# Kernel tuning notes

Hardware: AMD Instinct MI355X
Metric: run time of the kernel (lower is better)

Reference implementation:

```python
import jax, jax.numpy as jnp
import numpy as np

N_EMBD = 1024
N_HEAD = 16
HEAD_DIM = N_EMBD // N_HEAD


def setup_inputs() -> dict:
    key = jax.random.key(0)
    ks = jax.random.split(key, 5)
    scale = 0.02
    x = jax.random.normal(ks[0], (2, 2048, N_EMBD), dtype=jnp.float32)
    w_attn = jax.random.normal(ks[1], (N_EMBD, 3 * N_EMBD), dtype=jnp.float32) * scale
    b_attn = jax.random.normal(ks[2], (3 * N_EMBD,), dtype=jnp.float32) * scale
    w_proj = jax.random.normal(ks[3], (N_EMBD, N_EMBD), dtype=jnp.float32) * scale
    b_proj = jax.random.normal(ks[4], (N_EMBD,), dtype=jnp.float32) * scale
    return {"x": x, "w_attn": w_attn, "b_attn": b_attn, "w_proj": w_proj, "b_proj": b_proj}


def reference(x, w_attn, b_attn, w_proj, b_proj):
    B, T, C = x.shape
    qkv = x @ w_attn + b_attn  # [B,T,3C]
    q, k, v = jnp.split(qkv, 3, axis=-1)
    # [B, H, T, D]
    q = q.reshape(B, T, N_HEAD, HEAD_DIM).transpose(0, 2, 1, 3)
    k = k.reshape(B, T, N_HEAD, HEAD_DIM).transpose(0, 2, 1, 3)
    v = v.reshape(B, T, N_HEAD, HEAD_DIM).transpose(0, 2, 1, 3)
    att = jnp.einsum("bhqd,bhkd->bhqk", q, k) * (1.0 / np.sqrt(HEAD_DIM))
    causal = jnp.tril(jnp.ones((T, T), dtype=bool))
    att = jnp.where(causal[None, None], att, jnp.float32(-jnp.inf))
    att = jax.nn.softmax(att, axis=-1)
    y = jnp.einsum("bhqk,bhkd->bhqd", att, v)  # [B,H,T,D]
    y = y.transpose(0, 2, 1, 3).reshape(B, T, C)
    return y @ w_proj + b_proj
```

## Files before the change

### kernel.cpp

```cpp
#include <hip/hip_runtime.h>
#include <stdint.h>

#define SEQ   2048
#define EMBD  1024
#define M_ROWS 4096

typedef unsigned short u16;
typedef unsigned int u32;
typedef __attribute__((ext_vector_type(8))) short bf16x8;
typedef __attribute__((ext_vector_type(4))) float f32x4;

__device__ __forceinline__ u16 f2b(float f) {
  u32 x = __float_as_uint(f);
  return (u16)((x + 0x7FFFu + ((x >> 16) & 1u)) >> 16);
}

__device__ __forceinline__ u32 pkbf(float a, float b) {
  u32 r;
  asm("v_cvt_pk_bf16_f32 %0, %1, %2" : "=v"(r) : "v"(a), "v"(b));
  return r;
}

__device__ __forceinline__ float exp2fast(float x) {
#if __has_builtin(__builtin_amdgcn_exp2f)
  return __builtin_amdgcn_exp2f(x);
#else
  return __expf(x * 0.69314718f);
#endif
}

__device__ __forceinline__ float rcpfast(float x) {
#if __has_builtin(__builtin_amdgcn_rcpf)
  return __builtin_amdgcn_rcpf(x);
#else
  return 1.f / x;
#endif
}

#define AS1(p) ((const __attribute__((address_space(1))) void*)(uintptr_t)(p))
#define AS3(p) ((__attribute__((address_space(3))) void*)(uintptr_t)(p))

__global__ __launch_bounds__(256) void cvt_f32_bf16(
    const float* __restrict__ in, u16* __restrict__ out, int n8) {
  int i = blockIdx.x * 256 + threadIdx.x;
  if (i >= n8) return;
  const float4* p = (const float4*)in + 2 * (size_t)i;
  float4 a = p[0], b = p[1];
  uint4 o;
  o.x = (u32)f2b(a.x) | ((u32)f2b(a.y) << 16);
  o.y = (u32)f2b(a.z) | ((u32)f2b(a.w) << 16);
  o.z = (u32)f2b(b.x) | ((u32)f2b(b.y) << 16);
  o.w = (u32)f2b(b.z) | ((u32)f2b(b.w) << 16);
  ((uint4*)out)[i] = o;
}

__global__ __launch_bounds__(256) void transpose_cvt2(
    const float* __restrict__ wa, u16* __restrict__ wat,
    const float* __restrict__ wp, u16* __restrict__ wpt) {
  __shared__ float t[64][65];
  const int bxr = blockIdx.x;
  const float* w = (bxr < 48) ? wa : wp;
  u16* wt = (bxr < 48) ? wat : wpt;
  const int N = (bxr < 48) ? 3072 : 1024;
  const int bx = (bxr < 48) ? bxr : bxr - 48;
  const int K = 1024;
  const int n0 = bx * 64, k0 = blockIdx.y * 64;
  const int c = threadIdx.x & 63, r4 = threadIdx.x >> 6;
#pragma unroll
  for (int j = 0; j < 16; ++j) {
    const int r = j * 4 + r4;
    t[c][r] = w[(size_t)(k0 + r) * N + n0 + c];
  }
  __syncthreads();
#pragma unroll
  for (int j = 0; j < 16; ++j) {
    const int nr = j * 4 + r4;
    wt[(size_t)(n0 + nr) * K + k0 + c] = f2b(t[nr][c]);
  }
}

template <bool OUT_BF16>
__global__ __launch_bounds__(256) void gemm_kmajor(
    const u16* __restrict__ A, const u16* __restrict__ Bt,
    const float* __restrict__ bias, void* __restrict__ outp,
    int M, int N, int K, int nbx) {
  __shared__ __align__(16) u16 sm[2][2][128 * 32];

  const int nwg = gridDim.x;
  const int qq = nwg >> 3, rr = nwg & 7;
  const int xcd = blockIdx.x & 7, off = blockIdx.x >> 3;
  const int wgid = (xcd < rr ? xcd * (qq + 1) : rr * (qq + 1) + (xcd - rr) * qq) + off;
  const int bx = wgid % nbx, by = wgid / nbx;
  const int row0 = by * 128, col0 = bx * 128;

  const int tid = threadIdx.x;
  const int w = tid >> 6, lane = tid & 63;
  const int wrow = (w >> 1) * 64, wcol = (w & 1) * 64;

  f32x4 acc[4][4];
#pragma unroll
  for (int a = 0; a < 4; ++a)
#pragma unroll
    for (int b = 0; b < 4; ++b)
#pragma unroll
      for (int e = 0; e < 4; ++e) acc[a][b][e] = 0.f;

  const size_t Kb = (size_t)K * 2;

  auto stage = [&](int k0, int buf) {
#pragma unroll
    for (int c = 0; c < 4; ++c) {
      const int ch = w * 4 + c;
      const int i = ch & 7;
      const int rloc = i * 16 + (lane >> 2);
      const int kb = ((lane & 3) * 16) ^ ((rloc & 3) << 4);
      const u16* mat = (ch < 8) ? A : Bt;
      const int r0 = (ch < 8) ? row0 : col0;
      const char* src = (const char*)mat + (size_t)(r0 + rloc) * Kb + k0 * 2 + kb;
      char* dst = (char*)&sm[buf][(ch < 8) ? 0 : 1][0] + i * 1024;
      __builtin_amdgcn_global_load_lds(AS1(src), AS3(dst), 16, 0, 0);
    }
  };

  auto compute = [&](int buf) {
    bf16x8 af[4], bfr[4];
    const char* As = (const char*)&sm[buf][0][0];
    const char* Bs = (const char*)&sm[buf][1][0];
#pragma unroll
    for (int rb = 0; rb < 4; ++rb) {
      const int rl = wrow + rb * 16 + (lane & 15);
      const int kb2 = ((lane >> 4) * 16) ^ ((rl & 3) << 4);
      af[rb] = *(const bf16x8*)(As + rl * 64 + kb2);
    }
#pragma unroll
    for (int cb = 0; cb < 4; ++cb) {
      const int rl = wcol + cb * 16 + (lane & 15);
      const int kb2 = ((lane >> 4) * 16) ^ ((rl & 3) << 4);
      bfr[cb] = *(const bf16x8*)(Bs + rl * 64 + kb2);
    }
#pragma unroll
    for (int rb = 0; rb < 4; ++rb)
#pragma unroll
      for (int cb = 0; cb < 4; ++cb)
        acc[rb][cb] = __builtin_amdgcn_mfma_f32_16x16x32_bf16(
            af[rb], bfr[cb], acc[rb][cb], 0, 0, 0);
  };

  const int nt = K >> 5;
  stage(0, 0);
  int cur = 0;
  for (int t = 0; t < nt - 1; ++t) {
    __syncthreads();
    stage((t + 1) * 32, cur ^ 1);
    compute(cur);
    cur ^= 1;
  }
  __syncthreads();
  compute(cur);

#pragma unroll
  for (int cb = 0; cb < 4; ++cb) {
    const int colg = col0 + wcol + cb * 16 + (lane & 15);
    const float bv = bias[colg];
#pragma unroll
    for (int rb = 0; rb < 4; ++rb) {
#pragma unroll
      for (int i = 0; i < 4; ++i) {
        const int rowg = row0 + wrow + rb * 16 + (lane >> 4) * 4 + i;
        const float v = acc[rb][cb][i] + bv;
        if (OUT_BF16) {
          const u32 hv = f2b(v);
          const u32 pv = (u32)__shfl_xor((int)hv, 1);
          if (!(lane & 1))
            *(u32*)((u16*)outp + (size_t)rowg * N + colg) = hv | (pv << 16);
        } else {
          ((float*)outp)[(size_t)rowg * N + colg] = v;
        }
      }
    }
  }
}

__global__ __launch_bounds__(256, 2) void attn_mfma2(
    const u16* __restrict__ qkvb, u16* __restrict__ yb) {
  __shared__ __align__(16) char lds[32768];

  const int bx = blockIdx.x;
  const int pr = bx >> 5;
  const int bh = bx & 31;
  const int bb = bh >> 4, h = bh & 15;

  const int tid = threadIdx.x;
  const int w = tid >> 6, lane = tid & 63;
  const int hh = lane >> 4, qh = lane & 15;

  const size_t rowb = 6144;
  const char* base = (const char*)qkvb + (size_t)bb * SEQ * rowb;
  const int koffb = EMBD * 2 + h * 128;
  const int voffb = 2 * EMBD * 2 + h * 128;

  const int krow_in_chunk = lane >> 3;
  const int vkv = (tid & 31) * 2;
  const int vdg = tid >> 5;

  for (int half = 0; half < 2; ++half) {
    const int qt = half ? pr : 31 - pr;
    const int q_abs = qt * 64 + w * 16 + qh;
    const int qloc = w * 16 + qh;

    const char* qp = base + (size_t)q_abs * rowb + h * 128 + hh * 16;
    const bf16x8 qf0 = *(const bf16x8*)qp;
    const bf16x8 qf1 = *(const bf16x8*)(qp + 64);

    float m2 = -1e30f, l = 0.f;
    f32x4 of[4];
#pragma unroll
    for (int db = 0; db < 4; ++db)
#pragma unroll
      for (int e = 0; e < 4; ++e) of[db][e] = 0.f;

    {
#pragma unroll
      for (int cc = 0; cc < 2; ++cc) {
        const int i = w * 2 + cc;
        const int kvl = i * 8 + krow_in_chunk;
        const int gs = (lane & 7) ^ ((i & 3) | ((krow_in_chunk & 1) << 2));
        const char* src = base + (size_t)kvl * rowb + koffb + gs * 16;
        __builtin_amdgcn_global_load_lds(AS1(src), AS3(lds + i * 1024), 16, 0, 0);
      }
      const char* vp = base + (size_t)vkv * rowb + voffb + vdg * 16;
      uint4 va = *(const uint4*)vp;
      uint4 vb = *(const uint4*)(vp + rowb);
      union { uint4 q; u16 s[8]; } ua, ub;
      ua.q = va; ub.q = vb;
      u32* vt = (u32*)(lds + 16384);
#pragma unroll
      for (int e = 0; e < 8; ++e) {
        const int d = vdg * 8 + e;
        vt[d * 32 + ((vkv >> 1) ^ ((d & 7) << 2))] =
            (u32)ua.s[e] | ((u32)ub.s[e] << 16);
      }
    }
    __syncthreads();

    for (int kt = 0; kt <= qt; ++kt) {
      const int cur = kt & 1;
      const char* ksb = lds + cur * 8192;
      const char* vtb = lds + 16384 + cur * 8192;

      uint4 va, vb;
      const bool pref = (kt < qt);
      if (pref) {
#pragma unroll
        for (int cc = 0; cc < 2; ++cc) {
          const int i = w * 2 + cc;
          const int kvl = i * 8 + krow_in_chunk;
          const int gs = (lane & 7) ^ ((i & 3) | ((krow_in_chunk & 1) << 2));
          const char* src =
              base + (size_t)((kt + 1) * 64 + kvl) * rowb + koffb + gs * 16;
          __builtin_amdgcn_global_load_lds(
              AS1(src), AS3(lds + (cur ^ 1) * 8192 + i * 1024), 16, 0, 0);
        }
        const char* vp =
            base + (size_t)((kt + 1) * 64 + vkv) * rowb + voffb + vdg * 16;
        va = *(const uint4*)vp;
        vb = *(const uint4*)(vp + rowb);
      }

      f32x4 st[4];
      __builtin_amdgcn_s_setprio(1);
#pragma unroll
      for (int rb = 0; rb < 4; ++rb) {
#pragma unroll
        for (int e = 0; e < 4; ++e) st[rb][e] = 0.f;
        const int kv = 32 * (rb >> 1) + 8 * ((lane >> 2) & 3) + 4 * (rb & 1) +
                       (lane & 3);
        const int f = ((kv >> 3) & 3) | ((kv & 1) << 2);
        const char* rp = ksb + kv * 128;
        const bf16x8 k0 = *(const bf16x8*)(rp + ((hh * 16) ^ (f << 4)));
        const bf16x8 k1 = *(const bf16x8*)(rp + ((64 + hh * 16) ^ (f << 4)));
        st[rb] = __builtin_amdgcn_mfma_f32_16x16x32_bf16(k0, qf0, st[rb], 0, 0, 0);
        st[rb] = __builtin_amdgcn_mfma_f32_16x16x32_bf16(k1, qf1, st[rb], 0, 0, 0);
      }
      __builtin_amdgcn_s_setprio(0);

      const float C = 0.18033688f;
      float pmax = -3.0e38f;
      if (kt == qt) {
#pragma unroll
        for (int rb = 0; rb < 4; ++rb) {
          const int kvb = 32 * (rb >> 1) + 8 * hh + 4 * (rb & 1);
#pragma unroll
          for (int i = 0; i < 4; ++i) {
            float v = st[rb][i] * C;
            if (kvb + i > qloc) v = -3.0e38f;
            st[rb][i] = v;
            pmax = fmaxf(pmax, v);
          }
        }
      } else {
#pragma unroll
        for (int rb = 0; rb < 4; ++rb)
#pragma unroll
          for (int i = 0; i < 4; ++i) {
            const float v = st[rb][i] * C;
            st[rb][i] = v;
            pmax = fmaxf(pmax, v);
          }
      }
      pmax = fmaxf(pmax, __shfl_xor(pmax, 16));
      pmax = fmaxf(pmax, __shfl_xor(pmax, 32));

      if (__any(pmax > m2 + 5.f)) {
        const float mn = fmaxf(m2, pmax);
        const float al = exp2fast(m2 - mn);
        m2 = mn;
        l *= al;
#pragma unroll
        for (int db = 0; db < 4; ++db)
#pragma unroll
          for (int e = 0; e < 4; ++e) of[db][e] *= al;
      }

      float ls = 0.f;
#pragma unroll
      for (int rb = 0; rb < 4; ++rb)
#pragma unroll
        for (int i = 0; i < 4; ++i) {
          const float p = exp2fast(st[rb][i] - m2);
          st[rb][i] = p;
          ls += p;
        }
      ls += __shfl_xor(ls, 16);
      ls += __shfl_xor(ls, 32);
      l += ls;

      union { u32 wd[4]; bf16x8 v; } pf0, pf1;
      pf0.wd[0] = pkbf(st[0][0], st[0][1]);
      pf0.wd[1] = pkbf(st[0][2], st[0][3]);
      pf0.wd[2] = pkbf(st[1][0], st[1][1]);
      pf0.wd[3] = pkbf(st[1][2], st[1][3]);
      pf1.wd[0] = pkbf(st[2][0], st[2][1]);
      pf1.wd[1] = pkbf(st[2][2], st[2][3]);
      pf1.wd[2] = pkbf(st[3][0], st[3][1]);
      pf1.wd[3] = pkbf(st[3][2], st[3][3]);

      __builtin_amdgcn_s_setprio(1);
#pragma unroll
      for (int db = 0; db < 4; ++db) {
        const int d = db * 16 + qh;
        const int g = d & 7;
        const char* rp = vtb + d * 128;
        const bf16x8 v0 = *(const bf16x8*)(rp + ((hh * 16) ^ (g << 4)));
        const bf16x8 v1 = *(const bf16x8*)(rp + ((64 + hh * 16) ^ (g << 4)));
        of[db] = __builtin_amdgcn_mfma_f32_16x16x32_bf16(v0, pf0.v, of[db], 0, 0, 0);
        of[db] = __builtin_amdgcn_mfma_f32_16x16x32_bf16(v1, pf1.v, of[db], 0, 0, 0);
      }
      __builtin_amdgcn_s_setprio(0);

      if (pref) {
        union { uint4 q; u16 s[8]; } ua, ub;
        ua.q = va; ub.q = vb;
        u32* vt = (u32*)(lds + 16384 + (cur ^ 1) * 8192);
#pragma unroll
        for (int e = 0; e < 8; ++e) {
          const int d = vdg * 8 + e;
          vt[d * 32 + ((vkv >> 1) ^ ((d & 7) << 2))] =
              (u32)ua.s[e] | ((u32)ub.s[e] << 16);
        }
      }
      __syncthreads();
    }

    const float inv = rcpfast(l);
    u16* yrow = yb + (size_t)(bb * SEQ + q_abs) * EMBD + h * 64;
#pragma unroll
    for (int db = 0; db < 4; ++db) {
      const u32 w0 = pkbf(of[db][0] * inv, of[db][1] * inv);
      const u32 w1 = pkbf(of[db][2] * inv, of[db][3] * inv);
      *(u32*)(yrow + db * 16 + 4 * hh) = w0;
      *(u32*)(yrow + db * 16 + 4 * hh + 2) = w1;
    }
    __syncthreads();
  }
}

extern "C" void kernel_launch(void* const* d_in, const int* in_sizes, int n_in,
                              void* d_out, int out_size, void* d_ws,
                              size_t ws_size, hipStream_t stream) {
  const float* x      = (const float*)d_in[0];
  const float* w_attn = (const float*)d_in[1];
  const float* b_attn = (const float*)d_in[2];
  const float* w_proj = (const float*)d_in[3];
  const float* b_proj = (const float*)d_in[4];
  float* out = (float*)d_out;

  u16* xb   = (u16*)d_ws;
  u16* wat  = xb + (size_t)M_ROWS * EMBD;
  u16* wpt  = wat + (size_t)3 * EMBD * EMBD;
  u16* qkvb = wpt + (size_t)EMBD * EMBD;
  u16* yb   = qkvb + (size_t)M_ROWS * 3 * EMBD;

  cvt_f32_bf16<<<(M_ROWS * EMBD / 8 + 255) / 256, 256, 0, stream>>>(
      x, xb, M_ROWS * EMBD / 8);
  transpose_cvt2<<<dim3(64, 16), 256, 0, stream>>>(w_attn, wat, w_proj, wpt);

  gemm_kmajor<true><<<768, 256, 0, stream>>>(
      xb, wat, b_attn, qkvb, M_ROWS, 3 * EMBD, EMBD, 24);

  attn_mfma2<<<512, 256, 0, stream>>>(qkvb, yb);

  gemm_kmajor<false><<<256, 256, 0, stream>>>(
      yb, wpt, b_proj, out, M_ROWS, EMBD, EMBD, 8);
}
```

Baseline: 188.2 us.

## Split attention into one block per query tile with XCD-aware mapping; fuse prep kernels

The attention kernel now launches one block per (batch-head, query tile) instead of pairing two query tiles per block. Block indices are remapped so each XCD handles a fixed set of heads, which keeps K/V reuse within one L2, and launch bounds allow four blocks per CU. The x conversion and weight transpose kernels are merged into one launch. In exchange, causal work per block is no longer balanced, so scheduling depends on the hardware dispatching the imbalanced blocks well.

```diff
diff --git a/kernel.cpp b/kernel.cpp
--- a/kernel.cpp
+++ b/kernel.cpp
@@ -40,31 +40,42 @@
 #define AS1(p) ((const __attribute__((address_space(1))) void*)(uintptr_t)(p))
 #define AS3(p) ((__attribute__((address_space(3))) void*)(uintptr_t)(p))
 
-__global__ __launch_bounds__(256) void cvt_f32_bf16(
-    const float* __restrict__ in, u16* __restrict__ out, int n8) {
-  int i = blockIdx.x * 256 + threadIdx.x;
-  if (i >= n8) return;
-  const float4* p = (const float4*)in + 2 * (size_t)i;
-  float4 a = p[0], b = p[1];
-  uint4 o;
-  o.x = (u32)f2b(a.x) | ((u32)f2b(a.y) << 16);
-  o.y = (u32)f2b(a.z) | ((u32)f2b(a.w) << 16);
-  o.z = (u32)f2b(b.x) | ((u32)f2b(b.y) << 16);
-  o.w = (u32)f2b(b.z) | ((u32)f2b(b.w) << 16);
-  ((uint4*)out)[i] = o;
-}
-
-__global__ __launch_bounds__(256) void transpose_cvt2(
+__global__ __launch_bounds__(256) void prep(
+    const float* __restrict__ x, u16* __restrict__ xb,
     const float* __restrict__ wa, u16* __restrict__ wat,
     const float* __restrict__ wp, u16* __restrict__ wpt) {
   __shared__ float t[64][65];
-  const int bxr = blockIdx.x;
+  const int bx = blockIdx.x;
+  if (bx < 1024) {
+    const size_t idx = (size_t)bx * 256 + threadIdx.x;
+    const float4* p = (const float4*)x + 4 * idx;
+    uint4 o0, o1;
+    {
+      float4 a = p[0], b = p[1];
+      o0.x = (u32)f2b(a.x) | ((u32)f2b(a.y) << 16);
+      o0.y = (u32)f2b(a.z) | ((u32)f2b(a.w) << 16);
+      o0.z = (u32)f2b(b.x) | ((u32)f2b(b.y) << 16);
+      o0.w = (u32)f2b(b.z) | ((u32)f2b(b.w) << 16);
+    }
+    {
+      float4 a = p[2], b = p[3];
+      o1.x = (u32)f2b(a.x) | ((u32)f2b(a.y) << 16);
+      o1.y = (u32)f2b(a.z) | ((u32)f2b(a.w) << 16);
+      o1.z = (u32)f2b(b.x) | ((u32)f2b(b.y) << 16);
+      o1.w = (u32)f2b(b.z) | ((u32)f2b(b.w) << 16);
+    }
+    ((uint4*)xb)[2 * idx] = o0;
+    ((uint4*)xb)[2 * idx + 1] = o1;
+    return;
+  }
+  const int tt = bx - 1024;
+  const int bxr = tt & 63, by = tt >> 6;
   const float* w = (bxr < 48) ? wa : wp;
   u16* wt = (bxr < 48) ? wat : wpt;
   const int N = (bxr < 48) ? 3072 : 1024;
-  const int bx = (bxr < 48) ? bxr : bxr - 48;
+  const int bxt = (bxr < 48) ? bxr : bxr - 48;
   const int K = 1024;
-  const int n0 = bx * 64, k0 = blockIdx.y * 64;
+  const int n0 = bxt * 64, k0 = by * 64;
   const int c = threadIdx.x & 63, r4 = threadIdx.x >> 6;
 #pragma unroll
   for (int j = 0; j < 16; ++j) {
@@ -181,13 +192,15 @@
   }
 }
 
-__global__ __launch_bounds__(256, 2) void attn_mfma2(
+__global__ __launch_bounds__(256, 4) void attn_mfma2(
     const u16* __restrict__ qkvb, u16* __restrict__ yb) {
   __shared__ __align__(16) char lds[32768];
 
   const int bx = blockIdx.x;
-  const int pr = bx >> 5;
-  const int bh = bx & 31;
+  const int xcd = bx & 7, g = bx >> 3;
+  const int j = g >> 5, r = g & 31;
+  const int bh = xcd * 4 + j;
+  const int qt = (j & 1) ? r : 31 - r;
   const int bb = bh >> 4, h = bh & 15;
 
   const int tid = threadIdx.x;
@@ -203,37 +216,163 @@
   const int vkv = (tid & 31) * 2;
   const int vdg = tid >> 5;
 
-  for (int half = 0; half < 2; ++half) {
-    const int qt = half ? pr : 31 - pr;
-    const int q_abs = qt * 64 + w * 16 + qh;
-    const int qloc = w * 16 + qh;
-
-    const char* qp = base + (size_t)q_abs * rowb + h * 128 + hh * 16;
-    const bf16x8 qf0 = *(const bf16x8*)qp;
-    const bf16x8 qf1 = *(const bf16x8*)(qp + 64);
-
-    float m2 = -1e30f, l = 0.f;
-    f32x4 of[4];
-#pragma unroll
-    for (int db = 0; db < 4; ++db)
-#pragma unroll
-      for (int e = 0; e < 4; ++e) of[db][e] = 0.f;
-
-    {
+  const int q_abs = qt * 64 + w * 16 + qh;
+  const int qloc = w * 16 + qh;
+
+  const char* qp = base + (size_t)q_abs * rowb + h * 128 + hh * 16;
+  const bf16x8 qf0 = *(const bf16x8*)qp;
+  const bf16x8 qf1 = *(const bf16x8*)(qp + 64);
+
+  float m2 = -1e30f, l = 0.f;
+  f32x4 of[4];
+#pragma unroll
+  for (int db = 0; db < 4; ++db)
+#pragma unroll
+    for (int e = 0; e < 4; ++e) of[db][e] = 0.f;
+
+  {
+#pragma unroll
+    for (int cc = 0; cc < 2; ++cc) {
+      const int i = w * 2 + cc;
+      const int kvl = i * 8 + krow_in_chunk;
+      const int gs = (lane & 7) ^ ((i & 3) | ((krow_in_chunk & 1) << 2));
+      const char* src = base + (size_t)kvl * rowb + koffb + gs * 16;
+      __builtin_amdgcn_global_load_lds(AS1(src), AS3(lds + i * 1024), 16, 0, 0);
+    }
+    const char* vp = base + (size_t)vkv * rowb + voffb + vdg * 16;
+    uint4 va = *(const uint4*)vp;
+    uint4 vb = *(const uint4*)(vp + rowb);
+    union { uint4 q; u16 s[8]; } ua, ub;
+    ua.q = va; ub.q = vb;
+    u32* vt = (u32*)(lds + 16384);
+#pragma unroll
+    for (int e = 0; e < 8; ++e) {
+      const int d = vdg * 8 + e;
+      vt[d * 32 + ((vkv >> 1) ^ ((d & 7) << 2))] =
+          (u32)ua.s[e] | ((u32)ub.s[e] << 16);
+    }
+  }
+  __syncthreads();
+
+  for (int kt = 0; kt <= qt; ++kt) {
+    const int cur = kt & 1;
+    const char* ksb = lds + cur * 8192;
+    const char* vtb = lds + 16384 + cur * 8192;
+
+    uint4 va, vb;
+    const bool pref = (kt < qt);
+    if (pref) {
 #pragma unroll
       for (int cc = 0; cc < 2; ++cc) {
         const int i = w * 2 + cc;
         const int kvl = i * 8 + krow_in_chunk;
         const int gs = (lane & 7) ^ ((i & 3) | ((krow_in_chunk & 1) << 2));
-        const char* src = base + (size_t)kvl * rowb + koffb + gs * 16;
-        __builtin_amdgcn_global_load_lds(AS1(src), AS3(lds + i * 1024), 16, 0, 0);
+        const char* src =
+            base + (size_t)((kt + 1) * 64 + kvl) * rowb + koffb + gs * 16;
+        __builtin_amdgcn_global_load_lds(
+            AS1(src), AS3(lds + (cur ^ 1) * 8192 + i * 1024), 16, 0, 0);
       }
-      const char* vp = base + (size_t)vkv * rowb + voffb + vdg * 16;
-      uint4 va = *(const uint4*)vp;
-      uint4 vb = *(const uint4*)(vp + rowb);
+      const char* vp =
+          base + (size_t)((kt + 1) * 64 + vkv) * rowb + voffb + vdg * 16;
+      va = *(const uint4*)vp;
+      vb = *(const uint4*)(vp + rowb);
+    }
+
+    f32x4 st[4];
+    __builtin_amdgcn_s_setprio(1);
+#pragma unroll
+    for (int rb = 0; rb < 4; ++rb) {
+#pragma unroll
+      for (int e = 0; e < 4; ++e) st[rb][e] = 0.f;
+      const int kv = 32 * (rb >> 1) + 8 * ((lane >> 2) & 3) + 4 * (rb & 1) +
+                     (lane & 3);
+      const int f = ((kv >> 3) & 3) | ((kv & 1) << 2);
+      const char* rp = ksb + kv * 128;
+      const bf16x8 k0 = *(const bf16x8*)(rp + ((hh * 16) ^ (f << 4)));
+      const bf16x8 k1 = *(const bf16x8*)(rp + ((64 + hh * 16) ^ (f << 4)));
+      st[rb] = __builtin_amdgcn_mfma_f32_16x16x32_bf16(k0, qf0, st[rb], 0, 0, 0);
+      st[rb] = __builtin_amdgcn_mfma_f32_16x16x32_bf16(k1, qf1, st[rb], 0, 0, 0);
+    }
+    __builtin_amdgcn_s_setprio(0);
+
+    const float C = 0.18033688f;
+    float pmax = -3.0e38f;
+    if (kt == qt) {
+#pragma unroll
+      for (int rb = 0; rb < 4; ++rb) {
+        const int kvb = 32 * (rb >> 1) + 8 * hh + 4 * (rb & 1);
+#pragma unroll
+        for (int i = 0; i < 4; ++i) {
+          float v = st[rb][i] * C;
+          if (kvb + i > qloc) v = -3.0e38f;
+          st[rb][i] = v;
+          pmax = fmaxf(pmax, v);
+        }
+      }
+    } else {
+#pragma unroll
+      for (int rb = 0; rb < 4; ++rb)
+#pragma unroll
+        for (int i = 0; i < 4; ++i) {
+          const float v = st[rb][i] * C;
+          st[rb][i] = v;
+          pmax = fmaxf(pmax, v);
+        }
+    }
+    pmax = fmaxf(pmax, __shfl_xor(pmax, 16));
+    pmax = fmaxf(pmax, __shfl_xor(pmax, 32));
+
+    if (__any(pmax > m2 + 5.f)) {
+      const float mn = fmaxf(m2, pmax);
+      const float al = exp2fast(m2 - mn);
+      m2 = mn;
+      l *= al;
+#pragma unroll
+      for (int db = 0; db < 4; ++db)
+#pragma unroll
+        for (int e = 0; e < 4; ++e) of[db][e] *= al;
+    }
+
+    float ls = 0.f;
+#pragma unroll
+    for (int rb = 0; rb < 4; ++rb)
+#pragma unroll
+      for (int i = 0; i < 4; ++i) {
+        const float p = exp2fast(st[rb][i] - m2);
+        st[rb][i] = p;
+        ls += p;
+      }
+    ls += __shfl_xor(ls, 16);
+    ls += __shfl_xor(ls, 32);
+    l += ls;
+
+    union { u32 wd[4]; bf16x8 v; } pf0, pf1;
+    pf0.wd[0] = pkbf(st[0][0], st[0][1]);
+    pf0.wd[1] = pkbf(st[0][2], st[0][3]);
+    pf0.wd[2] = pkbf(st[1][0], st[1][1]);
+    pf0.wd[3] = pkbf(st[1][2], st[1][3]);
+    pf1.wd[0] = pkbf(st[2][0], st[2][1]);
+    pf1.wd[1] = pkbf(st[2][2], st[2][3]);
+    pf1.wd[2] = pkbf(st[3][0], st[3][1]);
+    pf1.wd[3] = pkbf(st[3][2], st[3][3]);
+
+    __builtin_amdgcn_s_setprio(1);
+#pragma unroll
+    for (int db = 0; db < 4; ++db) {
+      const int d = db * 16 + qh;
+      const int g2 = d & 7;
+      const char* rp = vtb + d * 128;
+      const bf16x8 v0 = *(const bf16x8*)(rp + ((hh * 16) ^ (g2 << 4)));
+      const bf16x8 v1 = *(const bf16x8*)(rp + ((64 + hh * 16) ^ (g2 << 4)));
+      of[db] = __builtin_amdgcn_mfma_f32_16x16x32_bf16(v0, pf0.v, of[db], 0, 0, 0);
+      of[db] = __builtin_amdgcn_mfma_f32_16x16x32_bf16(v1, pf1.v, of[db], 0, 0, 0);
+    }
+    __builtin_amdgcn_s_setprio(0);
+
+    if (pref) {
       union { uint4 q; u16 s[8]; } ua, ub;
       ua.q = va; ub.q = vb;
-      u32* vt = (u32*)(lds + 16384);
+      u32* vt = (u32*)(lds + 16384 + (cur ^ 1) * 8192);
 #pragma unroll
       for (int e = 0; e < 8; ++e) {
         const int d = vdg * 8 + e;
@@ -242,146 +381,16 @@
       }
     }
     __syncthreads();
-
-    for (int kt = 0; kt <= qt; ++kt) {
-      const int cur = kt & 1;
-      const char* ksb = lds + cur * 8192;
-      const char* vtb = lds + 16384 + cur * 8192;
-
-      uint4 va, vb;
-      const bool pref = (kt < qt);
-      if (pref) {
-#pragma unroll
-        for (int cc = 0; cc < 2; ++cc) {
-          const int i = w * 2 + cc;
-          const int kvl = i * 8 + krow_in_chunk;
-          const int gs = (lane & 7) ^ ((i & 3) | ((krow_in_chunk & 1) << 2));
-          const char* src =
-              base + (size_t)((kt + 1) * 64 + kvl) * rowb + koffb + gs * 16;
-          __builtin_amdgcn_global_load_lds(
-              AS1(src), AS3(lds + (cur ^ 1) * 8192 + i * 1024), 16, 0, 0);
-        }
-        const char* vp =
-            base + (size_t)((kt + 1) * 64 + vkv) * rowb + voffb + vdg * 16;
-        va = *(const uint4*)vp;
-        vb = *(const uint4*)(vp + rowb);
-      }
-
-      f32x4 st[4];
-      __builtin_amdgcn_s_setprio(1);
-#pragma unroll
-      for (int rb = 0; rb < 4; ++rb) {
-#pragma unroll
-        for (int e = 0; e < 4; ++e) st[rb][e] = 0.f;
-        const int kv = 32 * (rb >> 1) + 8 * ((lane >> 2) & 3) + 4 * (rb & 1) +
-                       (lane & 3);
-        const int f = ((kv >> 3) & 3) | ((kv & 1) << 2);
-        const char* rp = ksb + kv * 128;
-        const bf16x8 k0 = *(const bf16x8*)(rp + ((hh * 16) ^ (f << 4)));
-        const bf16x8 k1 = *(const bf16x8*)(rp + ((64 + hh * 16) ^ (f << 4)));
-        st[rb] = __builtin_amdgcn_mfma_f32_16x16x32_bf16(k0, qf0, st[rb], 0, 0, 0);
-        st[rb] = __builtin_amdgcn_mfma_f32_16x16x32_bf16(k1, qf1, st[rb], 0, 0, 0);
-      }
-      __builtin_amdgcn_s_setprio(0);
-
-      const float C = 0.18033688f;
-      float pmax = -3.0e38f;
-      if (kt == qt) {
-#pragma unroll
-        for (int rb = 0; rb < 4; ++rb) {
-          const int kvb = 32 * (rb >> 1) + 8 * hh + 4 * (rb & 1);
-#pragma unroll
-          for (int i = 0; i < 4; ++i) {
-            float v = st[rb][i] * C;
-            if (kvb + i > qloc) v = -3.0e38f;
-            st[rb][i] = v;
-            pmax = fmaxf(pmax, v);
-          }
-        }
-      } else {
-#pragma unroll
-        for (int rb = 0; rb < 4; ++rb)
-#pragma unroll
-          for (int i = 0; i < 4; ++i) {
-            const float v = st[rb][i] * C;
-            st[rb][i] = v;
-            pmax = fmaxf(pmax, v);
-          }
-      }
-      pmax = fmaxf(pmax, __shfl_xor(pmax, 16));
-      pmax = fmaxf(pmax, __shfl_xor(pmax, 32));
-
-      if (__any(pmax > m2 + 5.f)) {
-        const float mn = fmaxf(m2, pmax);
-        const float al = exp2fast(m2 - mn);
-        m2 = mn;
-        l *= al;
-#pragma unroll
-        for (int db = 0; db < 4; ++db)
-#pragma unroll
-          for (int e = 0; e < 4; ++e) of[db][e] *= al;
-      }
-
-      float ls = 0.f;
-#pragma unroll
-      for (int rb = 0; rb < 4; ++rb)
-#pragma unroll
-        for (int i = 0; i < 4; ++i) {
-          const float p = exp2fast(st[rb][i] - m2);
-          st[rb][i] = p;
-          ls += p;
-        }
-      ls += __shfl_xor(ls, 16);
-      ls += __shfl_xor(ls, 32);
-      l += ls;
-
-      union { u32 wd[4]; bf16x8 v; } pf0, pf1;
-      pf0.wd[0] = pkbf(st[0][0], st[0][1]);
-      pf0.wd[1] = pkbf(st[0][2], st[0][3]);
-      pf0.wd[2] = pkbf(st[1][0], st[1][1]);
-      pf0.wd[3] = pkbf(st[1][2], st[1][3]);
-      pf1.wd[0] = pkbf(st[2][0], st[2][1]);
-      pf1.wd[1] = pkbf(st[2][2], st[2][3]);
-      pf1.wd[2] = pkbf(st[3][0], st[3][1]);
-      pf1.wd[3] = pkbf(st[3][2], st[3][3]);
-
-      __builtin_amdgcn_s_setprio(1);
-#pragma unroll
-      for (int db = 0; db < 4; ++db) {
-        const int d = db * 16 + qh;
-        const int g = d & 7;
-        const char* rp = vtb + d * 128;
-        const bf16x8 v0 = *(const bf16x8*)(rp + ((hh * 16) ^ (g << 4)));
-        const bf16x8 v1 = *(const bf16x8*)(rp + ((64 + hh * 16) ^ (g << 4)));
-        of[db] = __builtin_amdgcn_mfma_f32_16x16x32_bf16(v0, pf0.v, of[db], 0, 0, 0);
-        of[db] = __builtin_amdgcn_mfma_f32_16x16x32_bf16(v1, pf1.v, of[db], 0, 0, 0);
-      }
-      __builtin_amdgcn_s_setprio(0);
-
-      if (pref) {
-        union { uint4 q; u16 s[8]; } ua, ub;
-        ua.q = va; ub.q = vb;
-        u32* vt = (u32*)(lds + 16384 + (cur ^ 1) * 8192);
-#pragma unroll
-        for (int e = 0; e < 8; ++e) {
-          const int d = vdg * 8 + e;
-          vt[d * 32 + ((vkv >> 1) ^ ((d & 7) << 2))] =
-              (u32)ua.s[e] | ((u32)ub.s[e] << 16);
-        }
-      }
-      __syncthreads();
-    }
-
-    const float inv = rcpfast(l);
-    u16* yrow = yb + (size_t)(bb * SEQ + q_abs) * EMBD + h * 64;
-#pragma unroll
-    for (int db = 0; db < 4; ++db) {
-      const u32 w0 = pkbf(of[db][0] * inv, of[db][1] * inv);
-      const u32 w1 = pkbf(of[db][2] * inv, of[db][3] * inv);
-      *(u32*)(yrow + db * 16 + 4 * hh) = w0;
-      *(u32*)(yrow + db * 16 + 4 * hh + 2) = w1;
-    }
-    __syncthreads();
+  }
+
+  const float inv = rcpfast(l);
+  u16* yrow = yb + (size_t)(bb * SEQ + q_abs) * EMBD + h * 64;
+#pragma unroll
+  for (int db = 0; db < 4; ++db) {
+    const u32 w0 = pkbf(of[db][0] * inv, of[db][1] * inv);
+    const u32 w1 = pkbf(of[db][2] * inv, of[db][3] * inv);
+    *(u32*)(yrow + db * 16 + 4 * hh) = w0;
+    *(u32*)(yrow + db * 16 + 4 * hh + 2) = w1;
   }
 }
 
@@ -401,14 +410,12 @@
   u16* qkvb = wpt + (size_t)EMBD * EMBD;
   u16* yb   = qkvb + (size_t)M_ROWS * 3 * EMBD;
 
-  cvt_f32_bf16<<<(M_ROWS * EMBD / 8 + 255) / 256, 256, 0, stream>>>(
-      x, xb, M_ROWS * EMBD / 8);
-  transpose_cvt2<<<dim3(64, 16), 256, 0, stream>>>(w_attn, wat, w_proj, wpt);
+  prep<<<2048, 256, 0, stream>>>(x, xb, w_attn, wat, w_proj, wpt);
 
   gemm_kmajor<true><<<768, 256, 0, stream>>>(
       xb, wat, b_attn, qkvb, M_ROWS, 3 * EMBD, EMBD, 24);
 
-  attn_mfma2<<<512, 256, 0, stream>>>(qkvb, yb);
+  attn_mfma2<<<1024, 256, 0, stream>>>(qkvb, yb);
 
   gemm_kmajor<false><<<256, 256, 0, stream>>>(
       yb, wpt, b_proj, out, M_ROWS, EMBD, EMBD, 8);
```

New measurement: 184.5 us. 1.02x faster.
